# Kernel tuning notes

Measured on AMD Instinct MI355X. Metric: run time of the kernel, lower is better.

## Reference

```python
import jax, jax.numpy as jnp
import numpy as np

N, E, CIN, H = 100000, 1600000, 128, 128


def setup_inputs() -> dict:
    key = jax.random.key(0)
    ks = jax.random.split(key, 10)
    return {
        "x": jax.random.normal(ks[0], (N, CIN), dtype=jnp.float32),
        "edge_index": jax.random.randint(ks[1], (2, E), 0, N, dtype=jnp.int64),
        "edge_weight": jax.random.uniform(ks[2], (E,), dtype=jnp.float32),
        "h_prev": jax.random.normal(ks[3], (N, H), dtype=jnp.float32),
        "c_prev": jax.random.normal(ks[4], (N, H), dtype=jnp.float32),
        "Wx0": jax.random.normal(ks[5], (4, CIN, H), dtype=jnp.float32) * 0.05,
        "Wx1": jax.random.normal(ks[6], (4, CIN, H), dtype=jnp.float32) * 0.05,
        "Wh0": jax.random.normal(ks[7], (4, H, H), dtype=jnp.float32) * 0.05,
        "Wh1": jax.random.normal(ks[8], (4, H, H), dtype=jnp.float32) * 0.05,
        "bx": jnp.zeros((4, H), dtype=jnp.float32),
        "bh": jnp.zeros((4, H), dtype=jnp.float32),
    }


def _scaled_laplacian_norm(edge_index, edge_weight, n):
    # PyG ChebConv norm with lambda_max=2.0, sym normalization:
    # L_hat = 2L/lambda_max - I = -D^{-1/2} A D^{-1/2} (zero diagonal).
    src, dst = edge_index[0], edge_index[1]
    deg = jax.ops.segment_sum(edge_weight, src, num_segments=n)
    safe = jnp.where(deg > 0, deg, 1.0)
    dis = jnp.where(deg > 0, 1.0 / jnp.sqrt(safe), 0.0)  # deg_inv_sqrt, inf->0
    norm = -(dis[src] * edge_weight * dis[dst])
    return src, dst, norm


def _propagate(feat, src, dst, norm, n):
    # (L_hat @ feat)[i] = sum_{e: dst_e=i} norm_e * feat[src_e]
    return jax.ops.segment_sum(feat[src] * norm[:, None], dst, num_segments=n)


def reference(x, edge_index, edge_weight, h_prev, c_prev, Wx0, Wx1, Wh0, Wh1, bx, bh):
    n = x.shape[0]
    src, dst, norm = _scaled_laplacian_norm(edge_index, edge_weight, n)
    # Shared Chebyshev propagation across all 4 gates (K=2: T0=I, T1=L_hat)
    Lx = _propagate(x, src, dst, norm, n)          # [N, CIN]
    Lh = _propagate(h_prev, src, dst, norm, n)     # [N, H]
    gates = (
        jnp.einsum("nc,gch->gnh", x, Wx0)
        + jnp.einsum("nc,gch->gnh", Lx, Wx1)
        + jnp.einsum("nd,gdh->gnh", h_prev, Wh0)
        + jnp.einsum("nd,gdh->gnh", Lh, Wh1)
        + bx[:, None, :] + bh[:, None, :]
    )  # [4, N, H]
    i = jax.nn.sigmoid(gates[0])
    f = jax.nn.sigmoid(gates[1])
    g = jnp.tanh(gates[2])
    o = jax.nn.sigmoid(gates[3])
    c_t = f * c_prev + i * g
    h_t = o * jnp.tanh(c_t)
    return (h_t, c_t)
```

## Files before the change

### kernel.cpp

```cpp
#include <hip/hip_runtime.h>
#include <hip/hip_bf16.h>

#define NN   100000
#define NE   1600000
#define MPAD 100096

typedef __attribute__((ext_vector_type(8))) short bf16x8;
typedef __attribute__((ext_vector_type(4))) float f32x4;

#define OFF_DEG    0ull
#define OFF_CNT    400384ull
#define OFF_CUR    800768ull
#define OFF_ROWPTR 1201152ull
#define OFF_BSUM   1601664ull
#define OFF_CSR    1602176ull
#define OFF_XH     14402176ull
#define OFF_FP     65651328ull
#define OFF_WT     116900480ull
#define OFF_BIAS   117424768ull

__device__ __forceinline__ unsigned short f2bf(float f) {
    unsigned int u = __float_as_uint(f);
    u += 0x7fffu + ((u >> 16) & 1u);
    return (unsigned short)(u >> 16);
}
__device__ __forceinline__ float bf2f(unsigned short u) {
    return __uint_as_float(((unsigned int)u) << 16);
}
__device__ __forceinline__ float sigf(float x)  { return 1.f / (1.f + __expf(-x)); }
__device__ __forceinline__ float tanhf_(float x){ return 1.f - 2.f / (__expf(2.f * x) + 1.f); }

typedef __attribute__((address_space(3))) void lds_void;
typedef __attribute__((address_space(1))) void g_void;
__device__ __forceinline__ void gload16(const void* g, void* l) {
    __builtin_amdgcn_global_load_lds((const g_void*)g, (lds_void*)l, 16, 0, 0);
}

__global__ void zero_kernel(float4* __restrict__ p, int n4) {
    int t = blockIdx.x * 256 + threadIdx.x;
    if (t < n4) p[t] = make_float4(0.f, 0.f, 0.f, 0.f);
}

__global__ void deg_hist_kernel(const int* __restrict__ src, const int* __restrict__ dst,
                                const float* __restrict__ w,
                                float* __restrict__ deg, int* __restrict__ cnt) {
    int e = blockIdx.x * 256 + threadIdx.x;
    if (e >= NE) return;
    atomicAdd(&deg[src[e]], w[e]);
    atomicAdd(&cnt[dst[e]], 1);
}

__global__ void scan_part_kernel(const int* __restrict__ cnt, int* __restrict__ rowptr,
                                 int* __restrict__ bsum) {
    __shared__ int wsum[16];
    int t = threadIdx.x, lane = t & 63, w = t >> 6;
    int i = blockIdx.x * 1024 + t;
    int v = (i < NN) ? cnt[i] : 0;
    int s = v;
#pragma unroll
    for (int off = 1; off < 64; off <<= 1) {
        int u = __shfl_up(s, off, 64);
        if (lane >= off) s += u;
    }
    if (lane == 63) wsum[w] = s;
    __syncthreads();
    if (w == 0) {
        int ws = (lane < 16) ? wsum[lane] : 0;
#pragma unroll
        for (int off = 1; off < 16; off <<= 1) {
            int u = __shfl_up(ws, off, 64);
            if (lane >= off) ws += u;
        }
        if (lane < 16) wsum[lane] = ws;
    }
    __syncthreads();
    int wbase = (w == 0) ? 0 : wsum[w - 1];
    if (i < NN) rowptr[i] = wbase + s - v;
    if (t == 1023) bsum[blockIdx.x] = wsum[15];
}

__global__ void scan_top_kernel(int* __restrict__ bsum, int* __restrict__ rowptr) {
    if (threadIdx.x == 0) {
        int a = 0;
        for (int b = 0; b < 98; ++b) { int t = bsum[b]; bsum[b] = a; a += t; }
        rowptr[NN] = a;
    }
}

__global__ void scan_add_kernel(const int* __restrict__ bsum, int* __restrict__ rowptr) {
    int i = blockIdx.x * 1024 + threadIdx.x;
    if (i < NN) rowptr[i] += bsum[blockIdx.x];
}

__global__ void fill_kernel(const int* __restrict__ src, const int* __restrict__ dst,
                            const float* __restrict__ w, const float* __restrict__ deg,
                            const int* __restrict__ rowptr, int* __restrict__ cursor,
                            uint2* __restrict__ csr) {
    int e = blockIdx.x * 256 + threadIdx.x;
    if (e >= NE) return;
    int s = src[e], d = dst[e];
    float ds = deg[s], dd = deg[d];
    float a = ds > 0.f ? rsqrtf(ds) : 0.f;
    float b = dd > 0.f ? rsqrtf(dd) : 0.f;
    int pos = rowptr[d] + atomicAdd(&cursor[d], 1);
    uint2 v; v.x = (unsigned)s; v.y = __float_as_uint(-(a * w[e] * b));
    csr[pos] = v;
}

__global__ void cvt_kernel(const float* __restrict__ x, const float* __restrict__ hp,
                           unsigned short* __restrict__ XH) {
    int t = blockIdx.x * 256 + threadIdx.x;
    int n = t >> 6, q = t & 63;
    ushort4 o = make_ushort4(0, 0, 0, 0);
    if (n < NN) {
        const float* s = (q < 32) ? (x + (size_t)n * 128 + (q << 2))
                                  : (hp + (size_t)n * 128 + ((q - 32) << 2));
        float4 v = *(const float4*)s;
        o = make_ushort4(f2bf(v.x), f2bf(v.y), f2bf(v.z), f2bf(v.w));
    }
    *(ushort4*)(XH + (size_t)n * 256 + (q << 2)) = o;
}

__launch_bounds__(256)
__global__ void gather_pack_kernel(const int* __restrict__ rowptr,
                                   const uint2* __restrict__ csr,
                                   const unsigned short* __restrict__ XH,
                                   unsigned short* __restrict__ Fp) {
    int node = (blockIdx.x * 256 + threadIdx.x) >> 6;
    int lane = threadIdx.x & 63;
    if (node >= MPAD) return;
    const int c4 = lane << 2;
    unsigned short* Frow = Fp + (size_t)node * 256;
    if (node >= NN) {
        *(ushort4*)(Frow + c4) = make_ushort4(0, 0, 0, 0);
        return;
    }
    int lo = rowptr[node], hi = rowptr[node + 1];
    float4 acc = make_float4(0.f, 0.f, 0.f, 0.f);
    int e = lo;
    for (; e + 1 < hi; e += 2) {
        uint2 e0 = csr[e], e1 = csr[e + 1];
        ushort4 v0 = *(const ushort4*)(XH + (size_t)e0.x * 256 + c4);
        ushort4 v1 = *(const ushort4*)(XH + (size_t)e1.x * 256 + c4);
        float n0 = __uint_as_float(e0.y), n1 = __uint_as_float(e1.y);
        acc.x += n0 * bf2f(v0.x); acc.y += n0 * bf2f(v0.y);
        acc.z += n0 * bf2f(v0.z); acc.w += n0 * bf2f(v0.w);
        acc.x += n1 * bf2f(v1.x); acc.y += n1 * bf2f(v1.y);
        acc.z += n1 * bf2f(v1.z); acc.w += n1 * bf2f(v1.w);
    }
    if (e < hi) {
        uint2 e0 = csr[e];
        ushort4 v0 = *(const ushort4*)(XH + (size_t)e0.x * 256 + c4);
        float n0 = __uint_as_float(e0.y);
        acc.x += n0 * bf2f(v0.x); acc.y += n0 * bf2f(v0.y);
        acc.z += n0 * bf2f(v0.z); acc.w += n0 * bf2f(v0.w);
    }
    *(ushort4*)(Frow + c4) =
        make_ushort4(f2bf(acc.x), f2bf(acc.y), f2bf(acc.z), f2bf(acc.w));
}

__global__ void pack_w_kernel(const float* __restrict__ Wx0, const float* __restrict__ Wx1,
                              const float* __restrict__ Wh0, const float* __restrict__ Wh1,
                              const float* __restrict__ bx,  const float* __restrict__ bh,
                              unsigned short* __restrict__ Wt, float* __restrict__ bias) {
    int t = blockIdx.x * 256 + threadIdx.x;
    int col = t >> 9, k = t & 511;
    int h = col >> 2, g = col & 3;
    const float* W; int kk;
    if      (k < 128) { W = Wx0; kk = k; }
    else if (k < 256) { W = Wx1; kk = k - 128; }
    else if (k < 384) { W = Wh0; kk = k - 256; }
    else              { W = Wh1; kk = k - 384; }
    float v = W[((size_t)(g << 7) + kk) * 128 + h];
    Wt[(size_t)col * 512 + k] = f2bf(v);
    if (k == 0) bias[col] = bx[(g << 7) + h] + bh[(g << 7) + h];
}

__device__ __forceinline__ f32x4 shflx4(f32x4 v, int m) {
    f32x4 r;
    r[0] = __shfl_xor(v[0], m, 64);
    r[1] = __shfl_xor(v[1], m, 64);
    r[2] = __shfl_xor(v[2], m, 64);
    r[3] = __shfl_xor(v[3], m, 64);
    return r;
}
__device__ __forceinline__ float sel4(f32x4 v, int k) {
    float r = v[0];
    r = (k == 1) ? v[1] : r;
    r = (k == 2) ? v[2] : r;
    r = (k == 3) ? v[3] : r;
    return r;
}
__device__ __forceinline__ float pick4(float a0, float a1, float a2, float a3, int k) {
    float r = a0;
    r = (k == 1) ? a1 : r;
    r = (k == 2) ? a2 : r;
    r = (k == 3) ? a3 : r;
    return r;
}

__launch_bounds__(256)
__global__ void gemm_lstm_kernel(const unsigned short* __restrict__ XHu,
                                 const unsigned short* __restrict__ Fpu,
                                 const unsigned short* __restrict__ Wtu,
                                 const float* __restrict__ bias,
                                 const float* __restrict__ c_prev,
                                 float* __restrict__ out) {
    __shared__ __align__(16) short sa[2][128 * 32];
    __shared__ __align__(16) short sb[2][128 * 32];

    const int tid  = threadIdx.x;
    const int lane = tid & 63;
    const int wave = tid >> 6;
    const int wm = wave >> 1, wn = wave & 1;
    const int lr = lane & 15, lq = lane >> 4;

    const int b = blockIdx.x;
    const int ntile = (b >> 3) & 3;
    const int mtile = (b & 7) | ((b >> 5) << 3);
    if (mtile >= 782) return;
    const size_t m0 = (size_t)mtile * 128;
    const int n0 = ntile * 128;

    const short* XH = (const short*)XHu;
    const short* Fp = (const short*)Fpu;
    const short* Wt = (const short*)Wtu;

    const int arow = tid >> 2;
    const int ak   = (tid & 3) << 3;
    const size_t rowA = (m0 + arow) * 256 + ak;
    const short* gB0 = Wt + (size_t)(n0 + arow) * 512 + ak;
    const short* gB1 = gB0 + (size_t)64 * 512;

    const int rbase = wm * 64 + lq * 4 + (lr & 3);
    const int hbase = (n0 >> 2) + wn * 16 + (lr >> 2);
    float cp[4][4];
#pragma unroll
    for (int i = 0; i < 4; ++i) {
        size_t grow = m0 + rbase + i * 16;
#pragma unroll
        for (int j = 0; j < 4; ++j)
            cp[i][j] = (grow < NN) ? c_prev[grow * 128 + hbase + j * 4] : 0.f;
    }
    float bs[4];
#pragma unroll
    for (int j = 0; j < 4; ++j) bs[j] = bias[n0 + wn * 64 + j * 16 + lr];

    int offA[4], offB[4];
#pragma unroll
    for (int i = 0; i < 4; ++i) {
        offA[i] = (wm * 64 + i * 16 + lr) * 32 + lq * 8;
        offB[i] = (wn * 64 + i * 16 + lr) * 32 + lq * 8;
    }

    f32x4 acc[4][4];
#pragma unroll
    for (int i = 0; i < 4; ++i)
#pragma unroll
        for (int j = 0; j < 4; ++j) acc[i][j] = (f32x4){0.f, 0.f, 0.f, 0.f};

    auto stage = [&](int kt, int buf) {
        const int off = ((kt >> 3) << 7) + ((kt & 3) << 5);
        const short* Ab = ((kt >> 2) & 1) ? Fp : XH;
        gload16(Ab + rowA + off,              &sa[buf][wave * 512]);
        gload16(Ab + rowA + 64 * 256 + off,   &sa[buf][2048 + wave * 512]);
        gload16(gB0 + kt * 32, &sb[buf][wave * 512]);
        gload16(gB1 + kt * 32, &sb[buf][2048 + wave * 512]);
    };

    stage(0, 0);
    for (int kt = 0; kt < 16; ++kt) {
        __syncthreads();
        if (kt + 1 < 16) stage(kt + 1, (kt + 1) & 1);
        const int buf = kt & 1;
        bf16x8 af[4], bfr[4];
#pragma unroll
        for (int i = 0; i < 4; ++i) af[i]  = *(const bf16x8*)&sa[buf][offA[i]];
#pragma unroll
        for (int i = 0; i < 4; ++i) bfr[i] = *(const bf16x8*)&sb[buf][offB[i]];
#pragma unroll
        for (int i = 0; i < 4; ++i)
#pragma unroll
            for (int j = 0; j < 4; ++j)
                acc[i][j] = __builtin_amdgcn_mfma_f32_16x16x32_bf16(af[i], bfr[j], acc[i][j], 0, 0, 0);
    }

    const int k = lr & 3;
#pragma unroll
    for (int i = 0; i < 4; ++i) {
        size_t grow = m0 + rbase + i * 16;
        if (grow >= NN) continue;
#pragma unroll
        for (int j = 0; j < 4; ++j) {
            f32x4 v0 = acc[i][j];
            v0[0] += bs[j]; v0[1] += bs[j]; v0[2] += bs[j]; v0[3] += bs[j];
            f32x4 v1 = shflx4(v0, 1);
            f32x4 v2 = shflx4(v0, 2);
            f32x4 v3 = shflx4(v0, 3);
            float vv0 = sel4(v0, k), vv1 = sel4(v1, k),
                  vv2 = sel4(v2, k), vv3 = sel4(v3, k);
            float gi = pick4(vv0, vv1, vv2, vv3, k);
            float gf = pick4(vv0, vv1, vv2, vv3, k ^ 1);
            float gg = pick4(vv0, vv1, vv2, vv3, k ^ 2);
            float go = pick4(vv0, vv1, vv2, vv3, k ^ 3);
            float iv = sigf(gi), fv = sigf(gf), gv = tanhf_(gg), ov = sigf(go);
            float ct = fv * cp[i][j] + iv * gv;
            float ht = ov * tanhf_(ct);
            int h = hbase + j * 4;
            out[grow * 128 + h] = ht;
            out[(size_t)NN * 128 + grow * 128 + h] = ct;
        }
    }
}

extern "C" void kernel_launch(void* const* d_in, const int* in_sizes, int n_in,
                              void* d_out, int out_size, void* d_ws, size_t ws_size,
                              hipStream_t stream) {
    const float* x      = (const float*)d_in[0];
    const int*   ei     = (const int*)  d_in[1];
    const float* ew     = (const float*)d_in[2];
    const float* h_prev = (const float*)d_in[3];
    const float* c_prev = (const float*)d_in[4];
    const float* Wx0    = (const float*)d_in[5];
    const float* Wx1    = (const float*)d_in[6];
    const float* Wh0    = (const float*)d_in[7];
    const float* Wh1    = (const float*)d_in[8];
    const float* bx     = (const float*)d_in[9];
    const float* bh     = (const float*)d_in[10];
    float* out = (float*)d_out;

    char* ws = (char*)d_ws;
    float*          deg    = (float*)(ws + OFF_DEG);
    int*            cnt    = (int*)  (ws + OFF_CNT);
    int*            cursor = (int*)  (ws + OFF_CUR);
    int*            rowptr = (int*)  (ws + OFF_ROWPTR);
    int*            bsum   = (int*)  (ws + OFF_BSUM);
    uint2*          csr    = (uint2*)(ws + OFF_CSR);
    unsigned short* XH     = (unsigned short*)(ws + OFF_XH);
    unsigned short* Fp     = (unsigned short*)(ws + OFF_FP);
    unsigned short* Wt     = (unsigned short*)(ws + OFF_WT);
    float*          bias   = (float*)(ws + OFF_BIAS);

    const int* src = ei;
    const int* dst = ei + NE;

    zero_kernel<<<(75072 + 255) / 256, 256, 0, stream>>>((float4*)ws, 75072);

    deg_hist_kernel<<<NE / 256, 256, 0, stream>>>(src, dst, ew, deg, cnt);
    scan_part_kernel<<<98, 1024, 0, stream>>>(cnt, rowptr, bsum);
    scan_top_kernel<<<1, 64, 0, stream>>>(bsum, rowptr);
    scan_add_kernel<<<98, 1024, 0, stream>>>(bsum, rowptr);
    fill_kernel<<<NE / 256, 256, 0, stream>>>(src, dst, ew, deg, rowptr, cursor, csr);

    cvt_kernel<<<MPAD * 64 / 256, 256, 0, stream>>>(x, h_prev, XH);
    gather_pack_kernel<<<MPAD / 4, 256, 0, stream>>>(rowptr, csr, XH, Fp);
    pack_w_kernel<<<512 * 512 / 256, 256, 0, stream>>>(Wx0, Wx1, Wh0, Wh1, bx, bh, Wt, bias);

    gemm_lstm_kernel<<<3136, 256, 0, stream>>>(XH, Fp, Wt, bias, c_prev, out);
}
```

Before: 699.1 us.

## Widen SpMM gather loads, stream GEMM B operand from registers, fuse weight pack

Result: no change. 689.0 us (-1.4%).

```diff
diff --git a/kernel.cpp b/kernel.cpp
--- a/kernel.cpp
+++ b/kernel.cpp
@@ -7,6 +7,7 @@
 
 typedef __attribute__((ext_vector_type(8))) short bf16x8;
 typedef __attribute__((ext_vector_type(4))) float f32x4;
+typedef __attribute__((ext_vector_type(8))) unsigned short u16x8;
 
 #define OFF_DEG    0ull
 #define OFF_CNT    400384ull
@@ -107,18 +108,38 @@
     csr[pos] = v;
 }
 
-__global__ void cvt_kernel(const float* __restrict__ x, const float* __restrict__ hp,
-                           unsigned short* __restrict__ XH) {
-    int t = blockIdx.x * 256 + threadIdx.x;
-    int n = t >> 6, q = t & 63;
-    ushort4 o = make_ushort4(0, 0, 0, 0);
-    if (n < NN) {
-        const float* s = (q < 32) ? (x + (size_t)n * 128 + (q << 2))
-                                  : (hp + (size_t)n * 128 + ((q - 32) << 2));
-        float4 v = *(const float4*)s;
-        o = make_ushort4(f2bf(v.x), f2bf(v.y), f2bf(v.z), f2bf(v.w));
-    }
-    *(ushort4*)(XH + (size_t)n * 256 + (q << 2)) = o;
+#define CVT_BLOCKS 25024
+__global__ void cvt_packw_kernel(const float* __restrict__ x, const float* __restrict__ hp,
+                                 unsigned short* __restrict__ XH,
+                                 const float* __restrict__ Wx0, const float* __restrict__ Wx1,
+                                 const float* __restrict__ Wh0, const float* __restrict__ Wh1,
+                                 const float* __restrict__ bx,  const float* __restrict__ bh,
+                                 unsigned short* __restrict__ Wt, float* __restrict__ bias) {
+    int b = blockIdx.x;
+    if (b < CVT_BLOCKS) {
+        int t = b * 256 + threadIdx.x;
+        int n = t >> 6, q = t & 63;
+        ushort4 o = make_ushort4(0, 0, 0, 0);
+        if (n < NN) {
+            const float* s = (q < 32) ? (x + (size_t)n * 128 + (q << 2))
+                                      : (hp + (size_t)n * 128 + ((q - 32) << 2));
+            float4 v = *(const float4*)s;
+            o = make_ushort4(f2bf(v.x), f2bf(v.y), f2bf(v.z), f2bf(v.w));
+        }
+        *(ushort4*)(XH + (size_t)n * 256 + (q << 2)) = o;
+    } else {
+        int t = (b - CVT_BLOCKS) * 256 + threadIdx.x;
+        int col = t >> 9, k = t & 511;
+        int h = col >> 2, g = col & 3;
+        const float* W; int kk;
+        if      (k < 128) { W = Wx0; kk = k; }
+        else if (k < 256) { W = Wx1; kk = k - 128; }
+        else if (k < 384) { W = Wh0; kk = k - 256; }
+        else              { W = Wh1; kk = k - 384; }
+        float v = W[((size_t)(g << 7) + kk) * 128 + h];
+        Wt[(size_t)col * 512 + k] = f2bf(v);
+        if (k == 0) bias[col] = bx[(g << 7) + h] + bh[(g << 7) + h];
+    }
 }
 
 __launch_bounds__(256)
@@ -129,51 +150,41 @@
     int node = (blockIdx.x * 256 + threadIdx.x) >> 6;
     int lane = threadIdx.x & 63;
     if (node >= MPAD) return;
-    const int c4 = lane << 2;
+    const int g  = lane >> 4;
+    const int li = lane & 15;
     unsigned short* Frow = Fp + (size_t)node * 256;
     if (node >= NN) {
-        *(ushort4*)(Frow + c4) = make_ushort4(0, 0, 0, 0);
+        if (g < 2) *(uint4*)(Frow + li * 16 + g * 8) = make_uint4(0, 0, 0, 0);
         return;
     }
     int lo = rowptr[node], hi = rowptr[node + 1];
-    float4 acc = make_float4(0.f, 0.f, 0.f, 0.f);
-    int e = lo;
-    for (; e + 1 < hi; e += 2) {
-        uint2 e0 = csr[e], e1 = csr[e + 1];
-        ushort4 v0 = *(const ushort4*)(XH + (size_t)e0.x * 256 + c4);
-        ushort4 v1 = *(const ushort4*)(XH + (size_t)e1.x * 256 + c4);
-        float n0 = __uint_as_float(e0.y), n1 = __uint_as_float(e1.y);
-        acc.x += n0 * bf2f(v0.x); acc.y += n0 * bf2f(v0.y);
-        acc.z += n0 * bf2f(v0.z); acc.w += n0 * bf2f(v0.w);
-        acc.x += n1 * bf2f(v1.x); acc.y += n1 * bf2f(v1.y);
-        acc.z += n1 * bf2f(v1.z); acc.w += n1 * bf2f(v1.w);
-    }
-    if (e < hi) {
-        uint2 e0 = csr[e];
-        ushort4 v0 = *(const ushort4*)(XH + (size_t)e0.x * 256 + c4);
-        float n0 = __uint_as_float(e0.y);
-        acc.x += n0 * bf2f(v0.x); acc.y += n0 * bf2f(v0.y);
-        acc.z += n0 * bf2f(v0.z); acc.w += n0 * bf2f(v0.w);
-    }
-    *(ushort4*)(Frow + c4) =
-        make_ushort4(f2bf(acc.x), f2bf(acc.y), f2bf(acc.z), f2bf(acc.w));
-}
-
-__global__ void pack_w_kernel(const float* __restrict__ Wx0, const float* __restrict__ Wx1,
-                              const float* __restrict__ Wh0, const float* __restrict__ Wh1,
-                              const float* __restrict__ bx,  const float* __restrict__ bh,
-                              unsigned short* __restrict__ Wt, float* __restrict__ bias) {
-    int t = blockIdx.x * 256 + threadIdx.x;
-    int col = t >> 9, k = t & 511;
-    int h = col >> 2, g = col & 3;
-    const float* W; int kk;
-    if      (k < 128) { W = Wx0; kk = k; }
-    else if (k < 256) { W = Wx1; kk = k - 128; }
-    else if (k < 384) { W = Wh0; kk = k - 256; }
-    else              { W = Wh1; kk = k - 384; }
-    float v = W[((size_t)(g << 7) + kk) * 128 + h];
-    Wt[(size_t)col * 512 + k] = f2bf(v);
-    if (k == 0) bias[col] = bx[(g << 7) + h] + bh[(g << 7) + h];
+    float acc[16];
+#pragma unroll
+    for (int k = 0; k < 16; ++k) acc[k] = 0.f;
+
+    for (int e = lo + g; e < hi; e += 4) {
+        uint2 ce = csr[e];
+        const unsigned short* row = XH + (size_t)ce.x * 256 + li * 16;
+        u16x8 v0 = *(const u16x8*)(row);
+        u16x8 v1 = *(const u16x8*)(row + 8);
+        float nm = __uint_as_float(ce.y);
+#pragma unroll
+        for (int k = 0; k < 8; ++k) acc[k]     += nm * bf2f((unsigned short)v0[k]);
+#pragma unroll
+        for (int k = 0; k < 8; ++k) acc[k + 8] += nm * bf2f((unsigned short)v1[k]);
+    }
+#pragma unroll
+    for (int k = 0; k < 16; ++k) {
+        acc[k] += __shfl_xor(acc[k], 16, 64);
+        acc[k] += __shfl_xor(acc[k], 32, 64);
+    }
+    if (g < 2) {
+        u16x8 o;
+#pragma unroll
+        for (int k = 0; k < 8; ++k)
+            o[k] = f2bf((g & 1) ? acc[k + 8] : acc[k]);
+        *(u16x8*)(Frow + li * 16 + g * 8) = o;
+    }
 }
 
 __device__ __forceinline__ f32x4 shflx4(f32x4 v, int m) {
@@ -207,7 +218,6 @@
                                  const float* __restrict__ c_prev,
                                  float* __restrict__ out) {
     __shared__ __align__(16) short sa[2][128 * 32];
-    __shared__ __align__(16) short sb[2][128 * 32];
 
     const int tid  = threadIdx.x;
     const int lane = tid & 63;
@@ -229,11 +239,64 @@
     const int arow = tid >> 2;
     const int ak   = (tid & 3) << 3;
     const size_t rowA = (m0 + arow) * 256 + ak;
-    const short* gB0 = Wt + (size_t)(n0 + arow) * 512 + ak;
-    const short* gB1 = gB0 + (size_t)64 * 512;
+
+    const short* gBf = Wt + (size_t)(n0 + wn * 64 + lr) * 512 + lq * 8;
 
     const int rbase = wm * 64 + lq * 4 + (lr & 3);
     const int hbase = (n0 >> 2) + wn * 16 + (lr >> 2);
+    float bs[4];
+#pragma unroll
+    for (int j = 0; j < 4; ++j) bs[j] = bias[n0 + wn * 64 + j * 16 + lr];
+
+    int offA[4];
+#pragma unroll
+    for (int i = 0; i < 4; ++i)
+        offA[i] = (wm * 64 + i * 16 + lr) * 32 + lq * 8;
+
+    f32x4 acc[4][4];
+#pragma unroll
+    for (int i = 0; i < 4; ++i)
+#pragma unroll
+        for (int j = 0; j < 4; ++j) acc[i][j] = (f32x4){0.f, 0.f, 0.f, 0.f};
+
+    auto stageA = [&](int kt, int buf) {
+        const int off = ((kt >> 3) << 7) + ((kt & 3) << 5);
+        const short* Ab = ((kt >> 2) & 1) ? Fp : XH;
+        gload16(Ab + rowA + off,            &sa[buf][wave * 512]);
+        gload16(Ab + rowA + 64 * 256 + off, &sa[buf][2048 + wave * 512]);
+    };
+
+    bf16x8 bcur[4];
+#pragma unroll
+    for (int j = 0; j < 4; ++j)
+        bcur[j] = *(const bf16x8*)(gBf + (size_t)j * 8192);
+    stageA(0, 0);
+
+    for (int kt = 0; kt < 16; ++kt) {
+        __syncthreads();
+        const int buf = kt & 1;
+        if (kt < 15) stageA(kt + 1, buf ^ 1);
+        bf16x8 af[4];
+#pragma unroll
+        for (int i = 0; i < 4; ++i) af[i] = *(const bf16x8*)&sa[buf][offA[i]];
+        bf16x8 bn[4];
+        if (kt < 15) {
+            const short* bp = gBf + (kt + 1) * 32;
+#pragma unroll
+            for (int j = 0; j < 4; ++j)
+                bn[j] = *(const bf16x8*)(bp + (size_t)j * 8192);
+        }
+#pragma unroll
+        for (int i = 0; i < 4; ++i)
+#pragma unroll
+            for (int j = 0; j < 4; ++j)
+                acc[i][j] = __builtin_amdgcn_mfma_f32_16x16x32_bf16(af[i], bcur[j], acc[i][j], 0, 0, 0);
+        if (kt < 15) {
+#pragma unroll
+            for (int j = 0; j < 4; ++j) bcur[j] = bn[j];
+        }
+    }
+
     float cp[4][4];
 #pragma unroll
     for (int i = 0; i < 4; ++i) {
@@ -241,48 +304,6 @@
 #pragma unroll
         for (int j = 0; j < 4; ++j)
             cp[i][j] = (grow < NN) ? c_prev[grow * 128 + hbase + j * 4] : 0.f;
-    }
-    float bs[4];
-#pragma unroll
-    for (int j = 0; j < 4; ++j) bs[j] = bias[n0 + wn * 64 + j * 16 + lr];
-
-    int offA[4], offB[4];
-#pragma unroll
-    for (int i = 0; i < 4; ++i) {
-        offA[i] = (wm * 64 + i * 16 + lr) * 32 + lq * 8;
-        offB[i] = (wn * 64 + i * 16 + lr) * 32 + lq * 8;
-    }
-
-    f32x4 acc[4][4];
-#pragma unroll
-    for (int i = 0; i < 4; ++i)
-#pragma unroll
-        for (int j = 0; j < 4; ++j) acc[i][j] = (f32x4){0.f, 0.f, 0.f, 0.f};
-
-    auto stage = [&](int kt, int buf) {
-        const int off = ((kt >> 3) << 7) + ((kt & 3) << 5);
-        const short* Ab = ((kt >> 2) & 1) ? Fp : XH;
-        gload16(Ab + rowA + off,              &sa[buf][wave * 512]);
-        gload16(Ab + rowA + 64 * 256 + off,   &sa[buf][2048 + wave * 512]);
-        gload16(gB0 + kt * 32, &sb[buf][wave * 512]);
-        gload16(gB1 + kt * 32, &sb[buf][2048 + wave * 512]);
-    };
-
-    stage(0, 0);
-    for (int kt = 0; kt < 16; ++kt) {
-        __syncthreads();
-        if (kt + 1 < 16) stage(kt + 1, (kt + 1) & 1);
-        const int buf = kt & 1;
-        bf16x8 af[4], bfr[4];
-#pragma unroll
-        for (int i = 0; i < 4; ++i) af[i]  = *(const bf16x8*)&sa[buf][offA[i]];
-#pragma unroll
-        for (int i = 0; i < 4; ++i) bfr[i] = *(const bf16x8*)&sb[buf][offB[i]];
-#pragma unroll
-        for (int i = 0; i < 4; ++i)
-#pragma unroll
-            for (int j = 0; j < 4; ++j)
-                acc[i][j] = __builtin_amdgcn_mfma_f32_16x16x32_bf16(af[i], bfr[j], acc[i][j], 0, 0, 0);
     }
 
     const int k = lr & 3;
@@ -352,9 +373,10 @@
     scan_add_kernel<<<98, 1024, 0, stream>>>(bsum, rowptr);
     fill_kernel<<<NE / 256, 256, 0, stream>>>(src, dst, ew, deg, rowptr, cursor, csr);
 
-    cvt_kernel<<<MPAD * 64 / 256, 256, 0, stream>>>(x, h_prev, XH);
+    cvt_packw_kernel<<<CVT_BLOCKS + 1024, 256, 0, stream>>>(x, h_prev, XH,
+                                                            Wx0, Wx1, Wh0, Wh1, bx, bh,
+                                                            Wt, bias);
     gather_pack_kernel<<<MPAD / 4, 256, 0, stream>>>(rowptr, csr, XH, Fp);
-    pack_w_kernel<<<512 * 512 / 256, 256, 0, stream>>>(Wx0, Wx1, Wh0, Wh1, bx, bh, Wt, bias);
 
     gemm_lstm_kernel<<<3136, 256, 0, stream>>>(XH, Fp, Wt, bias, c_prev, out);
 }
```
